# Kernel optimization log

Measured on AMD Instinct MI355X. Metric: run time of the kernel, lower is better.

## Reference

```python
import math
import jax, jax.numpy as jnp
import numpy as np

B, T, D, H = 2, 2048, 1024, 16
N_LAYERS = 24


def get_slopes(n):
    def pow2(n):
        start = 2 ** (-2 ** (-(math.log2(n) - 3)))
        return [start * start ** i for i in range(n)]
    if math.log2(n).is_integer():
        return pow2(n)
    c = 2 ** math.floor(math.log2(n))
    return pow2(c) + get_slopes(2 * c)[0::2][: n - c]


def setup_inputs() -> dict:
    key = jax.random.key(0)
    ks = jax.random.split(key, 5)
    x = jax.random.normal(ks[0], (B, T, D), dtype=jnp.float32)
    Wq = 0.02 * jax.random.normal(ks[1], (D, D), dtype=jnp.float32)
    Wk = 0.02 * jax.random.normal(ks[2], (D, D), dtype=jnp.float32)
    Wv = 0.02 * jax.random.normal(ks[3], (D, D), dtype=jnp.float32)
    Wo = (0.02 / math.sqrt(2 * N_LAYERS)) * jax.random.normal(ks[4], (D, D), dtype=jnp.float32)
    z = jnp.zeros((D,), dtype=jnp.float32)
    return {"x": x, "Wq": Wq, "bq": z, "Wk": Wk, "bk": z, "Wv": Wv, "bv": z, "Wo": Wo, "bo": z}


def reference(x, Wq, bq, Wk, bk, Wv, bv, Wo, bo):
    Bb, Tt, C = x.shape
    hd = C // H
    # QKV projections -> (B, H, T, hd)
    q = (x @ Wq + bq).reshape(Bb, Tt, H, hd).transpose(0, 2, 1, 3)
    k = (x @ Wk + bk).reshape(Bb, Tt, H, hd).transpose(0, 2, 1, 3)
    v = (x @ Wv + bv).reshape(Bb, Tt, H, hd).transpose(0, 2, 1, 3)
    # scaled dot-product scores (B, H, T, T)
    attn = jnp.einsum('bhqd,bhkd->bhqk', q, k) / jnp.sqrt(jnp.asarray(hd, x.dtype))
    # ALiBi bias: module uses only last row of the relative-position matrix,
    # broadcast over query positions: -slope_h * (T-1 - j), shape (1, H, 1, T)
    slopes = jnp.asarray(get_slopes(H), dtype=x.dtype)
    alibi = -slopes[None, :, None, None] * (Tt - 1 - jnp.arange(Tt, dtype=x.dtype))[None, None, None, :]
    attn = attn + alibi
    # causal mask
    causal = jnp.tril(jnp.ones((Tt, Tt), dtype=bool))[None, None, :, :]
    attn = jnp.where(causal, attn, jnp.finfo(x.dtype).min)
    p = jax.nn.softmax(attn, axis=-1)
    out = jnp.einsum('bhqk,bhkd->bqhd', p, v).reshape(Bb, Tt, C)
    return out @ Wo + bo
```

## Files before the change

kernel.cpp:

```cpp
#include <hip/hip_runtime.h>
#include <hip/hip_bf16.h>

#define Bn 2
#define Tdim 2048
#define Ddim 1024
#define Hn 16
#define HD 64

typedef unsigned short u16;
typedef unsigned int u32;
typedef __attribute__((ext_vector_type(8))) __bf16 bf16x8;
typedef __attribute__((ext_vector_type(4))) float f32x4;
typedef __attribute__((ext_vector_type(16))) float f32x16;
typedef __attribute__((ext_vector_type(4))) u32 u32x4;

struct alignas(8) U16x4 { u16 x, y, z, w; };

__device__ __forceinline__ u16 f2bf(float f) {
  union { float f; u32 i; } v; v.f = f;
  u32 x = v.i;
  u32 r = (x + 0x7fffu + ((x >> 16) & 1u)) >> 16;
  return (u16)r;
}
__device__ __forceinline__ float bf2f(u16 u) {
  union { u32 i; float f; } v; v.i = ((u32)u) << 16; return v.f;
}

__device__ __forceinline__ u32 cvtpk_bf16(float a, float b) {
  u32 d;
  asm("v_cvt_pk_bf16_f32 %0, %1, %2" : "=v"(d) : "v"(a), "v"(b));
  return d;
}

__device__ __forceinline__ void cp16(const u16* g, u16* l) {
  __builtin_amdgcn_global_load_lds(
      (const __attribute__((address_space(1))) u32*)g,
      (__attribute__((address_space(3))) u32*)l, 16, 0, 0);
}

__device__ __forceinline__ f32x4 mfma16(bf16x8 a, bf16x8 b, f32x4 c) {
  return __builtin_amdgcn_mfma_f32_16x16x32_bf16(a, b, c, 0, 0, 0);
}
__device__ __forceinline__ f32x16 mfma32(bf16x8 a, bf16x8 b, f32x16 c) {
  return __builtin_amdgcn_mfma_f32_32x32x16_bf16(a, b, c, 0, 0, 0);
}

__global__ __launch_bounds__(256) void preproc_k(
    const float* __restrict__ x, u16* __restrict__ Xb,
    const float* __restrict__ s0, const float* __restrict__ s1,
    const float* __restrict__ s2, const float* __restrict__ s3,
    u16* __restrict__ dstW) {
  const int tx = threadIdx.x, ty = threadIdx.y;
  if (blockIdx.z == 4) {
    const int tid = ty * 32 + tx;
    const int i = ((blockIdx.y * 32 + blockIdx.x) * 256 + tid) * 16;
#pragma unroll
    for (int c = 0; c < 2; c++) {
      u16 t[8];
#pragma unroll
      for (int j = 0; j < 8; j++) t[j] = f2bf(x[i + c * 8 + j]);
      *(bf16x8*)&Xb[i + c * 8] = *(const bf16x8*)t;
    }
    return;
  }
  const float* src = (blockIdx.z == 0) ? s0 : (blockIdx.z == 1) ? s1
                   : (blockIdx.z == 2) ? s2 : s3;
  u16* d = dstW + (size_t)blockIdx.z * Ddim * Ddim;
  __shared__ u16 tile[32][33];
  const int xx = blockIdx.x * 32 + tx;
  const int y0 = blockIdx.y * 32;
#pragma unroll
  for (int j = 0; j < 32; j += 8) tile[ty + j][tx] = f2bf(src[(size_t)(y0 + ty + j) * Ddim + xx]);
  __syncthreads();
  const int xo = blockIdx.y * 32 + tx;
  const int yo0 = blockIdx.x * 32;
#pragma unroll
  for (int j = 0; j < 32; j += 8) d[(size_t)(yo0 + ty + j) * Ddim + xo] = tile[tx][ty + j];
}

__global__ __launch_bounds__(256, 2) void gemm_qkv(
    const u16* __restrict__ Xb, const u16* __restrict__ WT,
    const float* __restrict__ bq, const float* __restrict__ bk, const float* __restrict__ bv,
    u16* __restrict__ Q, u16* __restrict__ K, u16* __restrict__ Vt) {
  const int flat = blockIdx.x + 32 * (blockIdx.y + 8 * blockIdx.z);
  const int l = (flat & 7) * 96 + (flat >> 3);
  const int lbx = l & 31, lby = (l >> 5) & 7, z = l >> 8;

  const u16* Wt = WT + (size_t)z * Ddim * Ddim;
  const float* bias = (z == 0) ? bq : (z == 1) ? bk : bv;
  u16* QK = (z == 0) ? Q : K;

  __shared__ alignas(16) u16 Alds[128 * 64];
  __shared__ alignas(16) u16 Blds[128 * 64];
  const int tid = threadIdx.x;
  const int w = tid >> 6, lane = tid & 63, ln = lane & 15, quad = lane >> 4;
  const int wm = (w >> 1) * 64, wn = (w & 1) * 64;
  const int tm = lbx * 128, tn = lby * 128;

  f32x4 acc[4][4] = {};

  const int srow = lane >> 3;
  const int scol = ((lane & 7) ^ srow) * 8;
  const u16* ag0 = Xb + (size_t)(tm + w * 32 + srow) * Ddim + scol;
  const u16* bg0 = Wt + (size_t)(tn + w * 32 + srow) * Ddim + scol;

  for (int k0 = 0; k0 < Ddim; k0 += 64) {
    __syncthreads();
#pragma unroll
    for (int j = 0; j < 4; j++) {
      cp16(ag0 + (size_t)j * 8 * Ddim + k0, &Alds[(w * 32 + j * 8) * 64]);
      cp16(bg0 + (size_t)j * 8 * Ddim + k0, &Blds[(w * 32 + j * 8) * 64]);
    }
    __syncthreads();
#pragma unroll
    for (int k2 = 0; k2 < 2; k2++) {
      const int so = ((k2 * 4 + quad) ^ (ln & 7)) * 8;
      bf16x8 af[4], bfr[4];
#pragma unroll
      for (int i = 0; i < 4; i++)
        af[i] = *(const bf16x8*)&Alds[(wm + i * 16 + ln) * 64 + so];
#pragma unroll
      for (int i = 0; i < 4; i++)
        bfr[i] = *(const bf16x8*)&Blds[(wn + i * 16 + ln) * 64 + so];
#pragma unroll
      for (int mi = 0; mi < 4; mi++)
#pragma unroll
        for (int ni = 0; ni < 4; ni++)
          acc[mi][ni] = mfma16(af[mi], bfr[ni], acc[mi][ni]);
    }
  }

#pragma unroll
  for (int mi = 0; mi < 4; mi++) {
#pragma unroll
    for (int ni = 0; ni < 4; ni++) {
      const int gm0 = tm + wm + mi * 16 + quad * 4;
      const int gn = tn + wn + ni * 16 + ln;
      const float bv_ = bias[gn];
      const int hh = gn >> 6, dd = gn & 63;
      const int b0 = gm0 >> 11, t0 = gm0 & 2047;
      if (z < 2) {
        u16* p = QK + (((size_t)(b0 * Hn + hh) * Tdim) + t0) * HD + dd;
#pragma unroll
        for (int r = 0; r < 4; r++) p[r * HD] = f2bf(acc[mi][ni][r] + bv_);
      } else {
        U16x4 pk;
        pk.x = f2bf(acc[mi][ni][0] + bv_);
        pk.y = f2bf(acc[mi][ni][1] + bv_);
        pk.z = f2bf(acc[mi][ni][2] + bv_);
        pk.w = f2bf(acc[mi][ni][3] + bv_);
        *(U16x4*)&Vt[((size_t)(b0 * Hn + hh) * HD + dd) * Tdim + t0] = pk;
      }
    }
  }
}

#define KSTR 68
#define VSTR 132
#define L2E 1.44269504088896f
__global__ __launch_bounds__(256, 2) void attn_k(
    const u16* __restrict__ Q, const u16* __restrict__ K, const u16* __restrict__ Vt,
    u16* __restrict__ Op, float* __restrict__ lp) {
  __shared__ alignas(16) u16 Klds[128 * KSTR];
  __shared__ alignas(16) u16 Vtlds[64 * VSTR];

  const int id = blockIdx.x;
  const int xcd = id & 7, slot = id >> 3;
  const int bh = (xcd << 2) | (slot >> 4);
  const int inner = slot & 15;
  const int p = inner >> 1;
  const int s = inner & 1;
  const int tid = threadIdx.x;
  const int w = tid >> 6, lane = tid & 63;
  const int qi = lane & 31, hf = lane >> 5;

  const u16* Qh = Q + (size_t)bh * Tdim * HD;
  const u16* Kh = K + (size_t)bh * Tdim * HD;
  const u16* Vh = Vt + (size_t)bh * HD * Tdim;
  const float slope = exp2f(-0.5f * (float)((bh & 15) + 1));

  const float sl2 = slope * L2E;
  const float c1 = 0.125f * L2E;
  const float f4hf = (float)(4 * hf);
  float sg8[4], slm[4];
#pragma unroll
  for (int g = 0; g < 4; g++) sg8[g] = sl2 * (float)(8 * g);
#pragma unroll
  for (int m = 0; m < 4; m++) slm[m] = sl2 * (float)m;

  const int qbs[2] = {p, 15 - p};
  int K0[2], K1[2];
#pragma unroll
  for (int seg = 0; seg < 2; seg++) {
    const int nk = qbs[seg] + 1;
    const int h0 = (nk + 1) >> 1;
    K0[seg] = s ? h0 : 0;
    K1[seg] = s ? nk : h0;
  }

  bf16x8 kreg[4], vreg[4];
  {
    const int kb = ((K0[0] < K1[0]) ? K0[0] : K0[1]) * 128;
#pragma unroll
    for (int c = 0; c < 4; c++) {
      const int e = c * 2048 + tid * 8;
      kreg[c] = *(const bf16x8*)&Kh[(size_t)(kb + (e >> 6)) * HD + (e & 63)];
      vreg[c] = *(const bf16x8*)&Vh[(size_t)(e >> 7) * Tdim + kb + (e & 127)];
    }
  }

  for (int seg = 0; seg < 2; seg++) {
    const int qb = qbs[seg];
    const int kt0 = K0[seg], kt1 = K1[seg];
    const int nkt = qb + 1;
    const int q0 = qb * 128;
    const int tg = q0 + w * 32 + qi;
    const float tt2 = (slope * (float)tg + 3.0f) * L2E;

    bf16x8 qf[4];
#pragma unroll
    for (int kc = 0; kc < 4; kc++)
      qf[kc] = *(const bf16x8*)&Qh[(size_t)tg * HD + kc * 16 + hf * 8];

    float ls0 = 0.f, ls1 = 0.f;
    f32x16 oacc[2] = {};

    for (int kt = kt0; kt < kt1; kt++) {
      const int kb = kt * 128;
      __syncthreads();
#pragma unroll
      for (int c = 0; c < 4; c++) {
        const int e = c * 2048 + tid * 8;
        *(bf16x8*)&Klds[(e >> 6) * KSTR + (e & 63)] = kreg[c];
        *(bf16x8*)&Vtlds[(e >> 7) * VSTR + (e & 127)] = vreg[c];
      }
      __syncthreads();

      {
        const int nxt = (kt + 1 < kt1) ? (kt + 1) : ((seg == 0) ? K0[1] : -1);
        if (nxt >= 0) {
          const int kb2 = nxt * 128;
#pragma unroll
          for (int c = 0; c < 4; c++) {
            const int e = c * 2048 + tid * 8;
            kreg[c] = *(const bf16x8*)&Kh[(size_t)(kb2 + (e >> 6)) * HD + (e & 63)];
            vreg[c] = *(const bf16x8*)&Vh[(size_t)(e >> 7) * Tdim + kb2 + (e & 127)];
          }
        }
      }

      f32x16 st[4] = {};
      __builtin_amdgcn_s_setprio(1);
#pragma unroll
      for (int kc = 0; kc < 4; kc++) {
#pragma unroll
        for (int ni = 0; ni < 4; ni++) {
          bf16x8 kf = *(const bf16x8*)&Klds[(ni * 32 + qi) * KSTR + kc * 16 + hf * 8];
          st[ni] = mfma32(kf, qf[kc], st[ni]);
        }
      }
      __builtin_amdgcn_s_setprio(0);

      const bool diag = (kt == nkt - 1);
      const float fkb = (float)kb + f4hf;
      bf16x8 pfrag[8];
#pragma unroll
      for (int ni = 0; ni < 4; ni++) {
        const float cni = __builtin_fmaf(sl2, fkb + (float)(32 * ni), -tt2);
        float pv[16];
        if (!diag) {
#pragma unroll
          for (int ri = 0; ri < 16; ri++) {
            const float e = __builtin_fmaf(st[ni][ri], c1, cni + sg8[ri >> 2] + slm[ri & 3]);
            const float pp = __builtin_amdgcn_exp2f(e);
            if (ri & 1) ls1 += pp; else ls0 += pp;
            pv[ri] = pp;
          }
        } else {
#pragma unroll
          for (int ri = 0; ri < 16; ri++) {
            const int n = kb + ni * 32 + (ri & 3) + 8 * (ri >> 2) + 4 * hf;
            const float e = __builtin_fmaf(st[ni][ri], c1, cni + sg8[ri >> 2] + slm[ri & 3]);
            float pp = __builtin_amdgcn_exp2f(e);
            if (n > tg) pp = 0.f;
            if (ri & 1) ls1 += pp; else ls0 += pp;
            pv[ri] = pp;
          }
        }
        u32 pk[4][2];
#pragma unroll
        for (int g = 0; g < 4; g++) {
          pk[g][0] = cvtpk_bf16(pv[g * 4 + 0], pv[g * 4 + 1]);
          pk[g][1] = cvtpk_bf16(pv[g * 4 + 2], pv[g * 4 + 3]);
        }
#pragma unroll
        for (int a = 0; a < 2; a++) {
          const u32 snd0 = (hf == 0) ? pk[2 * a + 1][0] : pk[2 * a][0];
          const u32 snd1 = (hf == 0) ? pk[2 * a + 1][1] : pk[2 * a][1];
          const u32 rcv0 = (u32)__shfl_xor((int)snd0, 32);
          const u32 rcv1 = (u32)__shfl_xor((int)snd1, 32);
          u32x4 fr;
          fr.x = (hf == 0) ? pk[2 * a][0] : rcv0;
          fr.y = (hf == 0) ? pk[2 * a][1] : rcv1;
          fr.z = (hf == 0) ? rcv0 : pk[2 * a + 1][0];
          fr.w = (hf == 0) ? rcv1 : pk[2 * a + 1][1];
          pfrag[ni * 2 + a] = *(bf16x8*)&fr;
        }
      }

      __builtin_amdgcn_s_setprio(1);
#pragma unroll
      for (int kf16 = 0; kf16 < 8; kf16++) {
#pragma unroll
        for (int nd = 0; nd < 2; nd++) {
          bf16x8 vf = *(const bf16x8*)&Vtlds[(nd * 32 + qi) * VSTR + kf16 * 16 + hf * 8];
          oacc[nd] = mfma32(pfrag[kf16], vf, oacc[nd]);
        }
      }
      __builtin_amdgcn_s_setprio(0);
    }

    float lsum = ls0 + ls1;
    lsum += __shfl_xor(lsum, 32);
    if (hf == 0) lp[(size_t)s * 65536 + bh * Tdim + tg] = lsum;

    u16* Ob = Op + (size_t)s * (32u * Tdim * HD) + ((size_t)bh * Tdim) * HD;
#pragma unroll
    for (int nd = 0; nd < 2; nd++) {
#pragma unroll
      for (int ri = 0; ri < 16; ri++) {
        const int rq = (ri & 3) + 8 * (ri >> 2) + 4 * hf;
        const int t = q0 + w * 32 + rq;
        Ob[(size_t)t * HD + nd * 32 + qi] = f2bf(oacc[nd][ri]);
      }
    }
  }
}

__global__ __launch_bounds__(256, 2) void gemm_out(
    const u16* __restrict__ Op, const float* __restrict__ lp,
    const u16* __restrict__ WoT, const float* __restrict__ bo,
    float* __restrict__ C) {
  const int flat = blockIdx.x + 64 * blockIdx.y;
  const int c = flat & 7, j = flat >> 3;
  const int lbx = c * 8 + (j & 7);
  const int lby = j >> 3;

  __shared__ alignas(16) u16 Alds[64 * 64];
  __shared__ alignas(16) u16 Blds[128 * 64];
  const int tid = threadIdx.x;
  const int w = tid >> 6, lane = tid & 63, ln = lane & 15, quad = lane >> 4;
  const int tm = lbx * 64, tn = lby * 128;

  f32x4 acc[4][2] = {};

  const int srow = lane >> 3;
  const int scol = ((lane & 7) ^ srow) * 8;
  const u16* bg0 = WoT + (size_t)(tn + w * 32 + srow) * Ddim + scol;

  const int ar = tid >> 3;
  const int ac8 = tid & 7;
  const int row0 = tm + ar, row1 = tm + ar + 32;
  const int b0r = row0 >> 11, t0r = row0 & 2047;
  const int b1r = row1 >> 11, t1r = row1 & 2047;
  const size_t pstr = (size_t)32 * Tdim * HD;
  const int aslot = (ac8 ^ (ar & 7)) * 8;

  u32x4 a00, a01, a10, a11;
  float l0a, l0b, l1a, l1b;
#define LOADA(H)                                                              \
  {                                                                           \
    const int bh0 = b0r * Hn + (H), bh1 = b1r * Hn + (H);                     \
    const size_t o0 = ((size_t)bh0 * Tdim + t0r) * HD + ac8 * 8;              \
    const size_t o1 = ((size_t)bh1 * Tdim + t1r) * HD + ac8 * 8;              \
    a00 = *(const u32x4*)&Op[o0];                                             \
    a01 = *(const u32x4*)&Op[pstr + o0];                                      \
    a10 = *(const u32x4*)&Op[o1];                                             \
    a11 = *(const u32x4*)&Op[pstr + o1];                                      \
    l0a = lp[bh0 * Tdim + t0r]; l0b = lp[65536 + bh0 * Tdim + t0r];           \
    l1a = lp[bh1 * Tdim + t1r]; l1b = lp[65536 + bh1 * Tdim + t1r];           \
  }

  LOADA(0);

  for (int k0 = 0; k0 < Ddim; k0 += 64) {
    __syncthreads();
#pragma unroll
    for (int jj = 0; jj < 4; jj++)
      cp16(bg0 + (size_t)jj * 8 * Ddim + k0, &Blds[(w * 32 + jj * 8) * 64]);
    {
      const float inv0 = 1.0f / (l0a + l0b);
      const float inv1 = 1.0f / (l1a + l1b);
      u32x4 q0, q1;
#pragma unroll
      for (int jj = 0; jj < 4; jj++) {
        const float lo0 = bf2f((u16)(a00[jj] & 0xffffu)) + bf2f((u16)(a01[jj] & 0xffffu));
        const float hi0 = bf2f((u16)(a00[jj] >> 16)) + bf2f((u16)(a01[jj] >> 16));
        q0[jj] = cvtpk_bf16(lo0 * inv0, hi0 * inv0);
        const float lo1 = bf2f((u16)(a10[jj] & 0xffffu)) + bf2f((u16)(a11[jj] & 0xffffu));
        const float hi1 = bf2f((u16)(a10[jj] >> 16)) + bf2f((u16)(a11[jj] >> 16));
        q1[jj] = cvtpk_bf16(lo1 * inv1, hi1 * inv1);
      }
      *(u32x4*)&Alds[ar * 64 + aslot] = q0;
      *(u32x4*)&Alds[(ar + 32) * 64 + aslot] = q1;
    }
    __syncthreads();
    if (k0 + 64 < Ddim) LOADA((k0 >> 6) + 1);
#pragma unroll
    for (int k2 = 0; k2 < 2; k2++) {
      const int so = ((k2 * 4 + quad) ^ (ln & 7)) * 8;
      bf16x8 af[4], bfr[2];
#pragma unroll
      for (int i = 0; i < 4; i++)
        af[i] = *(const bf16x8*)&Alds[(i * 16 + ln) * 64 + so];
#pragma unroll
      for (int i = 0; i < 2; i++)
        bfr[i] = *(const bf16x8*)&Blds[(w * 32 + i * 16 + ln) * 64 + so];
#pragma unroll
      for (int mi = 0; mi < 4; mi++)
#pragma unroll
        for (int ni = 0; ni < 2; ni++)
          acc[mi][ni] = mfma16(af[mi], bfr[ni], acc[mi][ni]);
    }
  }
#undef LOADA

#pragma unroll
  for (int mi = 0; mi < 4; mi++) {
#pragma unroll
    for (int ni = 0; ni < 2; ni++) {
      const int gm0 = tm + mi * 16 + quad * 4;
      const int gn = tn + w * 32 + ni * 16 + ln;
      const float bv_ = bo[gn];
#pragma unroll
      for (int r = 0; r < 4; r++)
        C[(size_t)(gm0 + r) * Ddim + gn] = acc[mi][ni][r] + bv_;
    }
  }
}

extern "C" void kernel_launch(void* const* d_in, const int* in_sizes, int n_in,
                              void* d_out, int out_size, void* d_ws, size_t ws_size,
                              hipStream_t stream) {
  (void)in_sizes; (void)n_in; (void)out_size; (void)ws_size;
  const float* x  = (const float*)d_in[0];
  const float* Wq = (const float*)d_in[1];
  const float* bq = (const float*)d_in[2];
  const float* Wk = (const float*)d_in[3];
  const float* bk = (const float*)d_in[4];
  const float* Wv = (const float*)d_in[5];
  const float* bv = (const float*)d_in[6];
  const float* Wo = (const float*)d_in[7];
  const float* bo = (const float*)d_in[8];

  char* ws = (char*)d_ws;
  const size_t MB = 1024 * 1024;
  u16* WT   = (u16*)(ws + 0 * MB);
  u16* Qb   = (u16*)(ws + 8 * MB);
  u16* Kb   = (u16*)(ws + 16 * MB);
  u16* Vtb  = (u16*)(ws + 24 * MB);
  u16* Xb   = (u16*)(ws + 32 * MB);
  u16* Opart= (u16*)(ws + 40 * MB);
  float* lpart = (float*)(ws + 56 * MB);
  u16* WoT = WT + (size_t)3 * Ddim * Ddim;

  preproc_k<<<dim3(32, 32, 5), dim3(32, 8), 0, stream>>>(x, Xb, Wq, Wk, Wv, Wo, WT);
  gemm_qkv<<<dim3(32, 8, 3), 256, 0, stream>>>(Xb, WT, bq, bk, bv, Qb, Kb, Vtb);
  attn_k<<<dim3(512), 256, 0, stream>>>(Qb, Kb, Vtb, Opart, lpart);
  gemm_out<<<dim3(64, 8), 256, 0, stream>>>(Opart, lpart, WoT, bo, (float*)d_out);
}
```

Baseline: 180.4 us.

## Double-buffer K/V LDS tiles in attention and vectorize Q/K projection stores

The attention kernel now keeps two K and two V LDS buffers. The next tile is stored into the alternate buffer mid-iteration, which removes one __syncthreads per key tile and overlaps global-load latency with compute. The QKV GEMM swaps MFMA operand order for the Q/K outputs so each lane holds four consecutive head dims, allowing packed 8-byte stores instead of strided 2-byte stores. Doubled LDS use (about 68KB per block) may limit occupancy under the declared two blocks per SM.

```diff
diff --git a/kernel.cpp b/kernel.cpp
--- a/kernel.cpp
+++ b/kernel.cpp
@@ -104,46 +104,68 @@
   const u16* ag0 = Xb + (size_t)(tm + w * 32 + srow) * Ddim + scol;
   const u16* bg0 = Wt + (size_t)(tn + w * 32 + srow) * Ddim + scol;
 
-  for (int k0 = 0; k0 < Ddim; k0 += 64) {
-    __syncthreads();
-#pragma unroll
-    for (int j = 0; j < 4; j++) {
-      cp16(ag0 + (size_t)j * 8 * Ddim + k0, &Alds[(w * 32 + j * 8) * 64]);
-      cp16(bg0 + (size_t)j * 8 * Ddim + k0, &Blds[(w * 32 + j * 8) * 64]);
-    }
-    __syncthreads();
-#pragma unroll
-    for (int k2 = 0; k2 < 2; k2++) {
-      const int so = ((k2 * 4 + quad) ^ (ln & 7)) * 8;
-      bf16x8 af[4], bfr[4];
-#pragma unroll
-      for (int i = 0; i < 4; i++)
-        af[i] = *(const bf16x8*)&Alds[(wm + i * 16 + ln) * 64 + so];
-#pragma unroll
-      for (int i = 0; i < 4; i++)
-        bfr[i] = *(const bf16x8*)&Blds[(wn + i * 16 + ln) * 64 + so];
-#pragma unroll
-      for (int mi = 0; mi < 4; mi++)
-#pragma unroll
-        for (int ni = 0; ni < 4; ni++)
-          acc[mi][ni] = mfma16(af[mi], bfr[ni], acc[mi][ni]);
-    }
-  }
-
-#pragma unroll
-  for (int mi = 0; mi < 4; mi++) {
-#pragma unroll
-    for (int ni = 0; ni < 4; ni++) {
-      const int gm0 = tm + wm + mi * 16 + quad * 4;
-      const int gn = tn + wn + ni * 16 + ln;
-      const float bv_ = bias[gn];
-      const int hh = gn >> 6, dd = gn & 63;
-      const int b0 = gm0 >> 11, t0 = gm0 & 2047;
-      if (z < 2) {
-        u16* p = QK + (((size_t)(b0 * Hn + hh) * Tdim) + t0) * HD + dd;
-#pragma unroll
-        for (int r = 0; r < 4; r++) p[r * HD] = f2bf(acc[mi][ni][r] + bv_);
-      } else {
+#define QKV_KLOOP(MFMA_EXPR)                                                  \
+  for (int k0 = 0; k0 < Ddim; k0 += 64) {                                     \
+    __syncthreads();                                                          \
+    _Pragma("unroll")                                                         \
+    for (int j = 0; j < 4; j++) {                                             \
+      cp16(ag0 + (size_t)j * 8 * Ddim + k0, &Alds[(w * 32 + j * 8) * 64]);    \
+      cp16(bg0 + (size_t)j * 8 * Ddim + k0, &Blds[(w * 32 + j * 8) * 64]);    \
+    }                                                                         \
+    __syncthreads();                                                          \
+    _Pragma("unroll")                                                         \
+    for (int k2 = 0; k2 < 2; k2++) {                                          \
+      const int so = ((k2 * 4 + quad) ^ (ln & 7)) * 8;                        \
+      bf16x8 af[4], bfr[4];                                                   \
+      _Pragma("unroll")                                                       \
+      for (int i = 0; i < 4; i++)                                             \
+        af[i] = *(const bf16x8*)&Alds[(wm + i * 16 + ln) * 64 + so];          \
+      _Pragma("unroll")                                                       \
+      for (int i = 0; i < 4; i++)                                             \
+        bfr[i] = *(const bf16x8*)&Blds[(wn + i * 16 + ln) * 64 + so];         \
+      _Pragma("unroll")                                                       \
+      for (int mi = 0; mi < 4; mi++)                                          \
+        _Pragma("unroll")                                                     \
+        for (int ni = 0; ni < 4; ni++)                                        \
+          acc[mi][ni] = MFMA_EXPR;                                            \
+    }                                                                         \
+  }
+
+  if (z < 2) {
+    QKV_KLOOP(mfma16(bfr[ni], af[mi], acc[mi][ni]))
+    float bv4[4][4];
+#pragma unroll
+    for (int ni = 0; ni < 4; ni++)
+#pragma unroll
+      for (int r = 0; r < 4; r++)
+        bv4[ni][r] = bias[tn + wn + ni * 16 + quad * 4 + r];
+#pragma unroll
+    for (int mi = 0; mi < 4; mi++) {
+      const int gm = tm + wm + mi * 16 + ln;
+      const int b0 = gm >> 11, t0 = gm & 2047;
+#pragma unroll
+      for (int ni = 0; ni < 4; ni++) {
+        const int gnq = tn + wn + ni * 16 + quad * 4;
+        const int hh = gnq >> 6, dd = gnq & 63;
+        U16x4 pk;
+        pk.x = f2bf(acc[mi][ni][0] + bv4[ni][0]);
+        pk.y = f2bf(acc[mi][ni][1] + bv4[ni][1]);
+        pk.z = f2bf(acc[mi][ni][2] + bv4[ni][2]);
+        pk.w = f2bf(acc[mi][ni][3] + bv4[ni][3]);
+        *(U16x4*)&QK[((size_t)(b0 * Hn + hh) * Tdim + t0) * HD + dd] = pk;
+      }
+    }
+  } else {
+    QKV_KLOOP(mfma16(af[mi], bfr[ni], acc[mi][ni]))
+#pragma unroll
+    for (int mi = 0; mi < 4; mi++) {
+#pragma unroll
+      for (int ni = 0; ni < 4; ni++) {
+        const int gm0 = tm + wm + mi * 16 + quad * 4;
+        const int gn = tn + wn + ni * 16 + ln;
+        const float bv_ = bias[gn];
+        const int hh = gn >> 6, dd = gn & 63;
+        const int b0 = gm0 >> 11, t0 = gm0 & 2047;
         U16x4 pk;
         pk.x = f2bf(acc[mi][ni][0] + bv_);
         pk.y = f2bf(acc[mi][ni][1] + bv_);
@@ -153,6 +175,7 @@
       }
     }
   }
+#undef QKV_KLOOP
 }
 
 #define KSTR 68
@@ -161,8 +184,8 @@
 __global__ __launch_bounds__(256, 2) void attn_k(
     const u16* __restrict__ Q, const u16* __restrict__ K, const u16* __restrict__ Vt,
     u16* __restrict__ Op, float* __restrict__ lp) {
-  __shared__ alignas(16) u16 Klds[128 * KSTR];
-  __shared__ alignas(16) u16 Vtlds[64 * VSTR];
+  __shared__ alignas(16) u16 Klds[2][128 * KSTR];
+  __shared__ alignas(16) u16 Vtlds[2][64 * VSTR];
 
   const int id = blockIdx.x;
   const int xcd = id & 7, slot = id >> 3;
@@ -207,7 +230,14 @@
       kreg[c] = *(const bf16x8*)&Kh[(size_t)(kb + (e >> 6)) * HD + (e & 63)];
       vreg[c] = *(const bf16x8*)&Vh[(size_t)(e >> 7) * Tdim + kb + (e & 127)];
     }
-  }
+#pragma unroll
+    for (int c = 0; c < 4; c++) {
+      const int e = c * 2048 + tid * 8;
+      *(bf16x8*)&Klds[0][(e >> 6) * KSTR + (e & 63)] = kreg[c];
+      *(bf16x8*)&Vtlds[0][(e >> 7) * VSTR + (e & 127)] = vreg[c];
+    }
+  }
+  int cb = 0;
 
   for (int seg = 0; seg < 2; seg++) {
     const int qb = qbs[seg];
@@ -228,24 +258,15 @@
     for (int kt = kt0; kt < kt1; kt++) {
       const int kb = kt * 128;
       __syncthreads();
-#pragma unroll
-      for (int c = 0; c < 4; c++) {
-        const int e = c * 2048 + tid * 8;
-        *(bf16x8*)&Klds[(e >> 6) * KSTR + (e & 63)] = kreg[c];
-        *(bf16x8*)&Vtlds[(e >> 7) * VSTR + (e & 127)] = vreg[c];
-      }
-      __syncthreads();
-
-      {
-        const int nxt = (kt + 1 < kt1) ? (kt + 1) : ((seg == 0) ? K0[1] : -1);
-        if (nxt >= 0) {
-          const int kb2 = nxt * 128;
-#pragma unroll
-          for (int c = 0; c < 4; c++) {
-            const int e = c * 2048 + tid * 8;
-            kreg[c] = *(const bf16x8*)&Kh[(size_t)(kb2 + (e >> 6)) * HD + (e & 63)];
-            vreg[c] = *(const bf16x8*)&Vh[(size_t)(e >> 7) * Tdim + kb2 + (e & 127)];
-          }
+
+      const int nxt = (kt + 1 < kt1) ? (kt + 1) : ((seg == 0) ? K0[1] : -1);
+      if (nxt >= 0) {
+        const int kb2 = nxt * 128;
+#pragma unroll
+        for (int c = 0; c < 4; c++) {
+          const int e = c * 2048 + tid * 8;
+          kreg[c] = *(const bf16x8*)&Kh[(size_t)(kb2 + (e >> 6)) * HD + (e & 63)];
+          vreg[c] = *(const bf16x8*)&Vh[(size_t)(e >> 7) * Tdim + kb2 + (e & 127)];
         }
       }
 
@@ -255,7 +276,7 @@
       for (int kc = 0; kc < 4; kc++) {
 #pragma unroll
         for (int ni = 0; ni < 4; ni++) {
-          bf16x8 kf = *(const bf16x8*)&Klds[(ni * 32 + qi) * KSTR + kc * 16 + hf * 8];
+          bf16x8 kf = *(const bf16x8*)&Klds[cb][(ni * 32 + qi) * KSTR + kc * 16 + hf * 8];
           st[ni] = mfma32(kf, qf[kc], st[ni]);
         }
       }
@@ -308,16 +329,27 @@
         }
       }
 
+      if (nxt >= 0) {
+#pragma unroll
+        for (int c = 0; c < 4; c++) {
+          const int e = c * 2048 + tid * 8;
+          *(bf16x8*)&Klds[cb ^ 1][(e >> 6) * KSTR + (e & 63)] = kreg[c];
+          *(bf16x8*)&Vtlds[cb ^ 1][(e >> 7) * VSTR + (e & 127)] = vreg[c];
+        }
+      }
+
       __builtin_amdgcn_s_setprio(1);
 #pragma unroll
       for (int kf16 = 0; kf16 < 8; kf16++) {
 #pragma unroll
         for (int nd = 0; nd < 2; nd++) {
-          bf16x8 vf = *(const bf16x8*)&Vtlds[(nd * 32 + qi) * VSTR + kf16 * 16 + hf * 8];
+          bf16x8 vf = *(const bf16x8*)&Vtlds[cb][(nd * 32 + qi) * VSTR + kf16 * 16 + hf * 8];
           oacc[nd] = mfma32(pfrag[kf16], vf, oacc[nd]);
         }
       }
       __builtin_amdgcn_s_setprio(0);
+
+      cb ^= 1;
     }
 
     float lsum = ls0 + ls1;
```

New measurement: 181.2 us. About the same (+0.4%).
